# Kernel optimization log

Measured on AMD Instinct MI355X. Metric: run time of the kernel, lower is better.

## Reference

```python
import jax, jax.numpy as jnp
import numpy as np

A = 2
IMG_C = 3
IMG_H = 64
IMG_W = 96
N_OBJ = 5   # OBJS + STACKS with REMOVE_BG
B = 64
P = 4       # number of predicate nets
CONV_OUT = 32


def setup_inputs() -> dict:
    key = jax.random.key(0)
    k0, k1, k2, k3 = jax.random.split(key, 4)
    state = jax.random.normal(k0, (B, N_OBJ, IMG_C, IMG_H, IMG_W), jnp.float32)
    state_next = jax.random.normal(k1, (B, N_OBJ, IMG_C, IMG_H, IMG_W), jnp.float32)
    # uniform object count (structural max N=5) so tuple count is static
    n_obj = jnp.full((B,), N_OBJ, dtype=jnp.int32)
    temp = jnp.float32(0.5)
    # stacked params for the P predicate nets (conv + linear head)
    conv_w = jax.random.normal(k2, (P * CONV_OUT, A * IMG_C, 3, 3), jnp.float32) * 0.05
    conv_b = jnp.zeros((P * CONV_OUT,), jnp.float32)
    w2 = jax.random.normal(k3, (P, CONV_OUT), jnp.float32) * 0.1
    b2 = jnp.zeros((P,), jnp.float32)
    return {"state": state, "state_next": state_next, "conv_w": conv_w,
            "conv_b": conv_b, "w2": w2, "b2": b2, "n_obj": n_obj, "temp": temp}


def _build_tuples(s, n):
    # cartesian_prod(arange(n), arange(n)) -> ordered pairs (i, j)
    ii = jnp.repeat(jnp.arange(n), n)   # [n*n]
    jj = jnp.tile(jnp.arange(n), n)     # [n*n]
    a = s[:, ii]                        # [B, n*n, C, H, W]
    b = s[:, jj]
    t = jnp.concatenate([a, b], axis=2)             # [B, n*n, A*C, H, W]
    return t.reshape(-1, A * IMG_C, IMG_H, IMG_W)   # [B*n*n, 6, H, W]


def _predicates(t, conv_w, conv_b, w2, b2, temp):
    # fused conv over all P nets (stacked output channels)
    y = jax.lax.conv_general_dilated(
        t, conv_w, window_strides=(2, 2), padding='SAME',
        dimension_numbers=('NCHW', 'OIHW', 'NCHW'))
    y = jax.nn.relu(y + conv_b[None, :, None, None])
    y = y.mean(axis=(2, 3)).reshape(-1, P, CONV_OUT)   # [T, P, 32]
    logits = jnp.einsum('tpc,pc->tp', y, w2) + b2      # [T, P]
    return jax.nn.sigmoid(logits / temp)


def reference(state, state_next, conv_w, conv_b, w2, b2, n_obj, temp):
    n = N_OBJ  # uniform ragged case: all n_obj entries equal the max
    tuples = _build_tuples(state, n)
    tuples_next = _build_tuples(state_next, n)
    preds = _predicates(tuples, conv_w, conv_b, w2, b2, temp)
    preds_next = _predicates(tuples_next, conv_w, conv_b, w2, b2, temp)
    # adjacency: column per tuple, one-hot in the owning sample's row
    T = B * n * n
    adj = (jnp.arange(T)[None, :] // (n * n) == jnp.arange(B)[:, None]).astype(jnp.float32)
    return preds, preds_next, adj
```

## Files before the change

kernel.cpp:

```cpp
#include <hip/hip_runtime.h>
#include <math.h>

#define BQ 64
#define NOBJ 5
#define CIN 3
#define IMG_H 64
#define IMG_W 96
#define OH 32
#define OW 48
#define NPAIR 25
#define PP 4
#define CONV_OUT 32

#define NRG 16
#define NPOS 96
#define XK 32
#define X_U32 (NOBJ * NPOS * XK / 2)
#define X_UNITS (NOBJ * NPOS * 4)

#define NPRED (2 * 1600 * PP)
#define ADJ_N (BQ * 1600)
#define S_FLOATS (2 * BQ * NPAIR * PP)

typedef __fp16   h2 __attribute__((ext_vector_type(2)));
typedef _Float16 half8 __attribute__((ext_vector_type(8)));
typedef float    float4_ __attribute__((ext_vector_type(4)));
typedef unsigned int uint4_ __attribute__((ext_vector_type(4)));

__global__ __launch_bounds__(512) void conv_pair_fused(
    const float* __restrict__ state,
    const float* __restrict__ state_next,
    const float* __restrict__ conv_w,
    const float* __restrict__ conv_b,
    const float* __restrict__ w2,
    const float* __restrict__ b2,
    const float* __restrict__ temp,
    float* __restrict__ S,
    unsigned int* __restrict__ cnt,
    float* __restrict__ out)
{
    __shared__ __align__(16) unsigned int sX32[X_U32];
    __shared__ int islast;

    const int tid = threadIdx.x;
    const int rg  = blockIdx.x;
    const int b   = blockIdx.y;
    const int src = blockIdx.z;

    const float* g = (src == 0 ? state : state_next)
                   + (size_t)b * NOBJ * CIN * IMG_H * IMG_W;
    const int R0 = rg * 4;

    if (src == 1 && tid < 100) {
        int a  = (rg + NRG * b) * 100 + tid;
        int bb = a / 1600;
        int t  = a - bb * 1600;
        out[NPRED + a] = (t / NPAIR == bb) ? 1.0f : 0.0f;
    }

    const int wave = tid >> 6;
    const int lane = tid & 63;
    const int quad = lane >> 4;
    const int ocl  = lane & 15;

    const int mt  = wave;
    const int p   = mt >> 1;
    const int row = mt * 16 + ocl;

    half8 wa, wb;
    #pragma unroll
    for (int j = 0; j < 8; ++j) {
        int k = quad * 8 + j;
        float va = 0.f, vb = 0.f;
        if (k < 27) {
            va = conv_w[row * 54 + k];
            vb = conv_w[row * 54 + 27 + k];
        } else if (k == 27) {
            va = conv_b[row];
        }
        wa[j] = (_Float16)va;
        wb[j] = (_Float16)vb;
    }
    h2 w2h01, w2h23;
    {
        const float* wp = w2 + p * CONV_OUT + (mt & 1) * 16 + quad * 4;
        w2h01 = __builtin_amdgcn_cvt_pkrtz(wp[0], wp[1]);
        w2h23 = __builtin_amdgcn_cvt_pkrtz(wp[2], wp[3]);
    }

    {
        const int subk = tid & 3;
        int koff[8], khv[8], kwv[8];
        float padf[8];
        bool kval[8];
        #pragma unroll
        for (int j = 0; j < 8; ++j) {
            int k = subk * 8 + j;
            if (k < 27) {
                int ci = k / 9;
                int r9 = k - ci * 9;
                int kh = r9 / 3;
                int kw = r9 - kh * 3;
                koff[j] = ci * (IMG_H * IMG_W) + kh * IMG_W + kw;
                khv[j] = kh; kwv[j] = kw; kval[j] = true; padf[j] = 0.f;
            } else {
                koff[j] = 0; khv[j] = 0; kwv[j] = 0; kval[j] = false;
                padf[j] = (k == 27) ? 1.0f : 0.f;
            }
        }
        for (int u = tid; u < X_UNITS; u += 512) {
            int pl  = (u >> 2) % NPOS;
            int obj = u / (NPOS * 4);
            int rl  = (pl >= 48) ? 1 : 0;
            int pc  = pl - rl * 48;
            int gr0 = R0 + 2 * rl;
            int gc0 = 2 * pc;
            const float* gp = g + obj * (CIN * IMG_H * IMG_W) + gr0 * IMG_W + gc0;
            float fv[8];
            #pragma unroll
            for (int j = 0; j < 8; ++j) {
                float v = padf[j];
                if (kval[j] && (gr0 + khv[j] < IMG_H) && (gc0 + kwv[j] < IMG_W))
                    v = gp[koff[j]];
                fv[j] = v;
            }
            uint4_ w4;
            w4.x = __builtin_bit_cast(unsigned int, __builtin_amdgcn_cvt_pkrtz(fv[0], fv[1]));
            w4.y = __builtin_bit_cast(unsigned int, __builtin_amdgcn_cvt_pkrtz(fv[2], fv[3]));
            w4.z = __builtin_bit_cast(unsigned int, __builtin_amdgcn_cvt_pkrtz(fv[4], fv[5]));
            w4.w = __builtin_bit_cast(unsigned int, __builtin_amdgcn_cvt_pkrtz(fv[6], fv[7]));
            int swk = subk ^ ((pl >> 1) & 3);
            *(uint4_*)&sX32[(size_t)(obj * (NPOS * 16) + pl * 16 + swk * 4)] = w4;
        }
    }

    __syncthreads();

    const float4_ zero4 = {0.f, 0.f, 0.f, 0.f};
    const h2 hz = {(__fp16)0.f, (__fp16)0.f};

    float acc[NPAIR];
    #pragma unroll
    for (int q = 0; q < NPAIR; ++q) acc[q] = 0.f;

    #pragma unroll
    for (int nt = 0; nt < 6; ++nt) {
        const int rl  = nt / 3;
        const int c0  = (nt - rl * 3) * 16;
        const int pos = rl * 48 + c0 + ocl;
        const int sw  = (pos >> 1) & 3;
        const int sbase = pos * 16 + ((quad ^ sw) << 2);

        half8 xf[NOBJ];
        h2 ah01[NOBJ], ah23[NOBJ];
        #pragma unroll
        for (int obj = 0; obj < NOBJ; ++obj) {
            xf[obj] = *(const half8*)&sX32[sbase + obj * (NPOS * 16)];
            float4_ a = __builtin_amdgcn_mfma_f32_16x16x32_f16(wa, xf[obj], zero4, 0, 0, 0);
            ah01[obj] = __builtin_amdgcn_cvt_pkrtz(a[0], a[1]);
            ah23[obj] = __builtin_amdgcn_cvt_pkrtz(a[2], a[3]);
        }

        #pragma unroll
        for (int jo = 0; jo < NOBJ; ++jo) {
            float4_ bq = __builtin_amdgcn_mfma_f32_16x16x32_f16(wb, xf[jo], zero4, 0, 0, 0);
            h2 bh01 = __builtin_amdgcn_cvt_pkrtz(bq[0], bq[1]);
            h2 bh23 = __builtin_amdgcn_cvt_pkrtz(bq[2], bq[3]);
            #pragma unroll
            for (int i = 0; i < NOBJ; ++i) {
                h2 s0 = ah01[i] + bh01;
                h2 s1 = ah23[i] + bh23;
                s0 = __builtin_elementwise_max(s0, hz);
                s1 = __builtin_elementwise_max(s1, hz);
                float t0 = __builtin_amdgcn_fdot2(s0, w2h01, acc[i * NOBJ + jo], false);
                acc[i * NOBJ + jo] = __builtin_amdgcn_fdot2(s1, w2h23, t0, false);
            }
        }
    }

    float myv = 0.f;
    #pragma unroll
    for (int q = 0; q < NPAIR; ++q) {
        float rr = acc[q];
        #pragma unroll
        for (int off = 32; off > 0; off >>= 1)
            rr += __shfl_xor(rr, off, 64);
        if (lane == q) myv = rr;
    }

    const size_t sbidx = ((size_t)src * BQ + b);
    if (lane < NPAIR)
        atomicAdd(&S[(sbidx * NPAIR + lane) * PP + p], myv);

    __syncthreads();
    if (tid == 0) {
        unsigned int old = atomicAdd(&cnt[sbidx], 1u);
        islast = (old == NRG - 1);
    }
    __syncthreads();

    if (islast && tid < NPAIR * PP) {
        int pair = tid >> 2;
        int pp   = tid & 3;
        float s = __hip_atomic_load(&S[(sbidx * NPAIR + pair) * PP + pp],
                                    __ATOMIC_RELAXED, __HIP_MEMORY_SCOPE_AGENT);
        float logit = s * (1.0f / (OH * OW)) + b2[pp];
        float x = logit / temp[0];
        out[(size_t)src * 6400 + ((size_t)b * NPAIR + pair) * PP + pp] =
            1.0f / (1.0f + expf(-x));
    }
}

extern "C" void kernel_launch(void* const* d_in, const int* in_sizes, int n_in,
                              void* d_out, int out_size, void* d_ws, size_t ws_size,
                              hipStream_t stream)
{
    const float* state      = (const float*)d_in[0];
    const float* state_next = (const float*)d_in[1];
    const float* conv_w     = (const float*)d_in[2];
    const float* conv_b     = (const float*)d_in[3];
    const float* w2         = (const float*)d_in[4];
    const float* b2         = (const float*)d_in[5];
    const float* temp       = (const float*)d_in[7];

    float* out = (float*)d_out;
    float* S   = (float*)d_ws;
    unsigned int* cnt = (unsigned int*)(S + S_FLOATS);

    hipMemsetAsync(d_ws, 0, (S_FLOATS + 2 * BQ) * sizeof(float), stream);

    dim3 grid1(NRG, BQ, 2);
    conv_pair_fused<<<grid1, 512, 0, stream>>>(state, state_next, conv_w, conv_b,
                                               w2, b2, temp, S, cnt, out);
}
```

Measured before the change: 155.4 us.

## Overlap second output row's global loads with first row's MFMA compute

The im2col staging of two output rows into shared memory is split. The first row is staged and synchronized. The second row's global loads are then issued into registers before the first row's MFMA/pair-accumulation compute, and written to LDS afterwards. This is meant to hide global load latency behind compute, at the cost of extra registers (16 floats held across the compute phase) and an extra barrier.

Result: slower. 192.7 us (+24.0%).

```diff
diff --git a/kernel.cpp b/kernel.cpp
--- a/kernel.cpp
+++ b/kernel.cpp
@@ -13,13 +13,11 @@
 #define CONV_OUT 32
 
 #define NRG 16
-#define NPOS 96
-#define XK 32
-#define X_U32 (NOBJ * NPOS * XK / 2)
-#define X_UNITS (NOBJ * NPOS * 4)
+#define RPOS 48
+#define ROW_U32 (NOBJ * RPOS * 16)
+#define ROWU (NOBJ * RPOS * 4)
 
 #define NPRED (2 * 1600 * PP)
-#define ADJ_N (BQ * 1600)
 #define S_FLOATS (2 * BQ * NPAIR * PP)
 
 typedef __fp16   h2 __attribute__((ext_vector_type(2)));
@@ -39,7 +37,7 @@
     unsigned int* __restrict__ cnt,
     float* __restrict__ out)
 {
-    __shared__ __align__(16) unsigned int sX32[X_U32];
+    __shared__ __align__(16) unsigned int sX32[2 * ROW_U32];
     __shared__ int islast;
 
     const int tid = threadIdx.x;
@@ -88,33 +86,32 @@
         w2h23 = __builtin_amdgcn_cvt_pkrtz(wp[2], wp[3]);
     }
 
+    const int subk = tid & 3;
+    int koff[8], khv[8], kwv[8];
+    float padf[8];
+    bool kval[8];
+    #pragma unroll
+    for (int j = 0; j < 8; ++j) {
+        int k = subk * 8 + j;
+        if (k < 27) {
+            int ci = k / 9;
+            int r9 = k - ci * 9;
+            int kh = r9 / 3;
+            int kw = r9 - kh * 3;
+            koff[j] = ci * (IMG_H * IMG_W) + kh * IMG_W + kw;
+            khv[j] = kh; kwv[j] = kw; kval[j] = true; padf[j] = 0.f;
+        } else {
+            koff[j] = 0; khv[j] = 0; kwv[j] = 0; kval[j] = false;
+            padf[j] = (k == 27) ? 1.0f : 0.f;
+        }
+    }
+
     {
-        const int subk = tid & 3;
-        int koff[8], khv[8], kwv[8];
-        float padf[8];
-        bool kval[8];
-        #pragma unroll
-        for (int j = 0; j < 8; ++j) {
-            int k = subk * 8 + j;
-            if (k < 27) {
-                int ci = k / 9;
-                int r9 = k - ci * 9;
-                int kh = r9 / 3;
-                int kw = r9 - kh * 3;
-                koff[j] = ci * (IMG_H * IMG_W) + kh * IMG_W + kw;
-                khv[j] = kh; kwv[j] = kw; kval[j] = true; padf[j] = 0.f;
-            } else {
-                koff[j] = 0; khv[j] = 0; kwv[j] = 0; kval[j] = false;
-                padf[j] = (k == 27) ? 1.0f : 0.f;
-            }
-        }
-        for (int u = tid; u < X_UNITS; u += 512) {
-            int pl  = (u >> 2) % NPOS;
-            int obj = u / (NPOS * 4);
-            int rl  = (pl >= 48) ? 1 : 0;
-            int pc  = pl - rl * 48;
-            int gr0 = R0 + 2 * rl;
-            int gc0 = 2 * pc;
+        const int gr0 = R0;
+        for (int u = tid; u < ROWU; u += 512) {
+            int pl  = (u >> 2) % RPOS;
+            int obj = u / (RPOS * 4);
+            int gc0 = 2 * pl;
             const float* gp = g + obj * (CIN * IMG_H * IMG_W) + gr0 * IMG_W + gc0;
             float fv[8];
             #pragma unroll
@@ -130,11 +127,49 @@
             w4.z = __builtin_bit_cast(unsigned int, __builtin_amdgcn_cvt_pkrtz(fv[4], fv[5]));
             w4.w = __builtin_bit_cast(unsigned int, __builtin_amdgcn_cvt_pkrtz(fv[6], fv[7]));
             int swk = subk ^ ((pl >> 1) & 3);
-            *(uint4_*)&sX32[(size_t)(obj * (NPOS * 16) + pl * 16 + swk * 4)] = w4;
+            *(uint4_*)&sX32[(size_t)(obj * (RPOS * 16) + pl * 16 + swk * 4)] = w4;
         }
     }
 
     __syncthreads();
+
+    float fvA[8], fvB[8];
+    bool hasB;
+    {
+        const int gr1 = R0 + 2;
+        {
+            int u   = tid;
+            int pl  = (u >> 2) % RPOS;
+            int obj = u / (RPOS * 4);
+            int gc0 = 2 * pl;
+            const float* gp = g + obj * (CIN * IMG_H * IMG_W) + gr1 * IMG_W + gc0;
+            #pragma unroll
+            for (int j = 0; j < 8; ++j) {
+                float v = padf[j];
+                if (kval[j] && (gr1 + khv[j] < IMG_H) && (gc0 + kwv[j] < IMG_W))
+                    v = gp[koff[j]];
+                fvA[j] = v;
+            }
+        }
+        hasB = (tid + 512 < ROWU);
+        if (hasB) {
+            int u   = tid + 512;
+            int pl  = (u >> 2) % RPOS;
+            int obj = u / (RPOS * 4);
+            int gc0 = 2 * pl;
+            const float* gp = g + obj * (CIN * IMG_H * IMG_W) + gr1 * IMG_W + gc0;
+            #pragma unroll
+            for (int j = 0; j < 8; ++j) {
+                float v = padf[j];
+                if (kval[j] && (gr1 + khv[j] < IMG_H) && (gc0 + kwv[j] < IMG_W))
+                    v = gp[koff[j]];
+                fvB[j] = v;
+            }
+        } else {
+            #pragma unroll
+            for (int j = 0; j < 8; ++j) fvB[j] = 0.f;
+        }
+    }
 
     const float4_ zero4 = {0.f, 0.f, 0.f, 0.f};
     const h2 hz = {(__fp16)0.f, (__fp16)0.f};
@@ -143,40 +178,71 @@
     #pragma unroll
     for (int q = 0; q < NPAIR; ++q) acc[q] = 0.f;
 
-    #pragma unroll
-    for (int nt = 0; nt < 6; ++nt) {
-        const int rl  = nt / 3;
-        const int c0  = (nt - rl * 3) * 16;
-        const int pos = rl * 48 + c0 + ocl;
-        const int sw  = (pos >> 1) & 3;
-        const int sbase = pos * 16 + ((quad ^ sw) << 2);
-
-        half8 xf[NOBJ];
-        h2 ah01[NOBJ], ah23[NOBJ];
-        #pragma unroll
-        for (int obj = 0; obj < NOBJ; ++obj) {
-            xf[obj] = *(const half8*)&sX32[sbase + obj * (NPOS * 16)];
-            float4_ a = __builtin_amdgcn_mfma_f32_16x16x32_f16(wa, xf[obj], zero4, 0, 0, 0);
-            ah01[obj] = __builtin_amdgcn_cvt_pkrtz(a[0], a[1]);
-            ah23[obj] = __builtin_amdgcn_cvt_pkrtz(a[2], a[3]);
-        }
-
-        #pragma unroll
-        for (int jo = 0; jo < NOBJ; ++jo) {
-            float4_ bq = __builtin_amdgcn_mfma_f32_16x16x32_f16(wb, xf[jo], zero4, 0, 0, 0);
-            h2 bh01 = __builtin_amdgcn_cvt_pkrtz(bq[0], bq[1]);
-            h2 bh23 = __builtin_amdgcn_cvt_pkrtz(bq[2], bq[3]);
-            #pragma unroll
-            for (int i = 0; i < NOBJ; ++i) {
-                h2 s0 = ah01[i] + bh01;
-                h2 s1 = ah23[i] + bh23;
-                s0 = __builtin_elementwise_max(s0, hz);
-                s1 = __builtin_elementwise_max(s1, hz);
-                float t0 = __builtin_amdgcn_fdot2(s0, w2h01, acc[i * NOBJ + jo], false);
-                acc[i * NOBJ + jo] = __builtin_amdgcn_fdot2(s1, w2h23, t0, false);
-            }
-        }
-    }
+    #define COMPUTE_ROW(RBASE)                                                   \
+    _Pragma("unroll")                                                            \
+    for (int nt3 = 0; nt3 < 3; ++nt3) {                                          \
+        const int pos = nt3 * 16 + ocl;                                          \
+        const int sw  = (pos >> 1) & 3;                                          \
+        const int sbase = (RBASE) + pos * 16 + ((quad ^ sw) << 2);               \
+        half8 xf[NOBJ];                                                          \
+        h2 ah01[NOBJ], ah23[NOBJ];                                               \
+        _Pragma("unroll")                                                        \
+        for (int obj = 0; obj < NOBJ; ++obj) {                                   \
+            xf[obj] = *(const half8*)&sX32[sbase + obj * (RPOS * 16)];           \
+            float4_ a = __builtin_amdgcn_mfma_f32_16x16x32_f16(wa, xf[obj], zero4, 0, 0, 0); \
+            ah01[obj] = __builtin_amdgcn_cvt_pkrtz(a[0], a[1]);                  \
+            ah23[obj] = __builtin_amdgcn_cvt_pkrtz(a[2], a[3]);                  \
+        }                                                                        \
+        _Pragma("unroll")                                                        \
+        for (int jo = 0; jo < NOBJ; ++jo) {                                      \
+            float4_ bq = __builtin_amdgcn_mfma_f32_16x16x32_f16(wb, xf[jo], zero4, 0, 0, 0); \
+            h2 bh01 = __builtin_amdgcn_cvt_pkrtz(bq[0], bq[1]);                  \
+            h2 bh23 = __builtin_amdgcn_cvt_pkrtz(bq[2], bq[3]);                  \
+            _Pragma("unroll")                                                    \
+            for (int i = 0; i < NOBJ; ++i) {                                     \
+                h2 s0 = ah01[i] + bh01;                                          \
+                h2 s1 = ah23[i] + bh23;                                          \
+                s0 = __builtin_elementwise_max(s0, hz);                          \
+                s1 = __builtin_elementwise_max(s1, hz);                          \
+                float t0 = __builtin_amdgcn_fdot2(s0, w2h01, acc[i * NOBJ + jo], false); \
+                acc[i * NOBJ + jo] = __builtin_amdgcn_fdot2(s1, w2h23, t0, false);       \
+            }                                                                    \
+        }                                                                        \
+    }
+
+    COMPUTE_ROW(0)
+
+    {
+        {
+            int u   = tid;
+            int pl  = (u >> 2) % RPOS;
+            int obj = u / (RPOS * 4);
+            uint4_ w4;
+            w4.x = __builtin_bit_cast(unsigned int, __builtin_amdgcn_cvt_pkrtz(fvA[0], fvA[1]));
+            w4.y = __builtin_bit_cast(unsigned int, __builtin_amdgcn_cvt_pkrtz(fvA[2], fvA[3]));
+            w4.z = __builtin_bit_cast(unsigned int, __builtin_amdgcn_cvt_pkrtz(fvA[4], fvA[5]));
+            w4.w = __builtin_bit_cast(unsigned int, __builtin_amdgcn_cvt_pkrtz(fvA[6], fvA[7]));
+            int swk = subk ^ ((pl >> 1) & 3);
+            *(uint4_*)&sX32[(size_t)(ROW_U32 + obj * (RPOS * 16) + pl * 16 + swk * 4)] = w4;
+        }
+        if (hasB) {
+            int u   = tid + 512;
+            int pl  = (u >> 2) % RPOS;
+            int obj = u / (RPOS * 4);
+            uint4_ w4;
+            w4.x = __builtin_bit_cast(unsigned int, __builtin_amdgcn_cvt_pkrtz(fvB[0], fvB[1]));
+            w4.y = __builtin_bit_cast(unsigned int, __builtin_amdgcn_cvt_pkrtz(fvB[2], fvB[3]));
+            w4.z = __builtin_bit_cast(unsigned int, __builtin_amdgcn_cvt_pkrtz(fvB[4], fvB[5]));
+            w4.w = __builtin_bit_cast(unsigned int, __builtin_amdgcn_cvt_pkrtz(fvB[6], fvB[7]));
+            int swk = subk ^ ((pl >> 1) & 3);
+            *(uint4_*)&sX32[(size_t)(ROW_U32 + obj * (RPOS * 16) + pl * 16 + swk * 4)] = w4;
+        }
+    }
+
+    __syncthreads();
+
+    COMPUTE_ROW(ROW_U32)
+    #undef COMPUTE_ROW
 
     float myv = 0.f;
     #pragma unroll
```
